# Performance work log

Measured on AMD Instinct MI355X. Metric: run time of the kernel, lower is better.

The kernel has to match this reference:

```python
import jax, jax.numpy as jnp
import numpy as np

T, D_IN, D_OUT, HEADS, FREQ = 2048, 1024, 1024, 8, 10000
DH = D_OUT // HEADS


def absolute_pos(t, d, freq):
    # AP[pos, 2i] = sin(pos / freq**(2i/d)), AP[pos, 2i+1] = cos(...); t even -> all cols filled
    pos = jnp.arange(t, dtype=jnp.float32)[:, None]            # [T,1]
    i = jnp.arange(t // 2, dtype=jnp.float32)[None, :]         # [1,T/2]
    angle = pos / (freq ** (2.0 * i / d))                      # [T,T/2]
    return jnp.stack([jnp.sin(angle), jnp.cos(angle)], axis=-1).reshape(t, t)


def setup_inputs() -> dict:
    key = jax.random.key(0)
    ks = jax.random.split(key, 6)
    s = 0.02
    return {
        "x": jax.random.normal(ks[0], (T, D_IN), jnp.float32),
        "Wq": jax.random.normal(ks[1], (HEADS, DH, D_IN), jnp.float32) * s,
        "Wk": jax.random.normal(ks[2], (HEADS, DH, D_IN), jnp.float32) * s,
        "Wv": jax.random.normal(ks[3], (HEADS, DH, D_IN), jnp.float32) * s,
        "Wout2": jax.random.normal(ks[4], (DH, DH + 2), jnp.float32) * s,
        "Wout": jax.random.normal(ks[5], (D_IN, D_OUT), jnp.float32) * s,
    }


def reference(x, Wq, Wk, Wv, Wout2, Wout):
    t = x.shape[0]
    # diversity = 1 - cosine similarity (F.normalize with eps=1e-12)
    x_unit = x / jnp.maximum(jnp.linalg.norm(x, axis=1, keepdims=True), 1e-12)
    diversity = 1.0 - x_unit @ x_unit.T                        # [T,T]

    # all heads vectorized; torch Linear weight is [out,in] -> x @ W.T
    Q = jnp.einsum('td,hed->hte', x, Wq)                       # [H,T,DH]
    K = jnp.einsum('td,hed->hte', x, Wk)
    V = jnp.einsum('td,hed->hte', x, Wv)

    AP = absolute_pos(t, D_IN, FREQ)                           # [T,T]
    energies = jnp.einsum('hte,hse->hts', Q, K) + AP           # [H,T,T]

    att = jax.nn.softmax(energies, axis=-1)
    logp = jax.nn.log_softmax(energies, axis=-1)
    entropy = -(att * logp).sum(-1) / np.float32(np.log(t))    # [H,T]
    entropy = entropy / jnp.maximum(jnp.abs(entropy).sum(-1, keepdims=True), 1e-12)

    # dep_factor[j] broadcast over rows: masked[i,j] = dep[j]*att[i,j]
    dep = (diversity[None] * att).sum(-1) / diversity.sum(-1)[None]  # [H,T]
    att_win = att + dep[:, None, :] * att                      # [H,T,T]

    # dropout(p=0.5) treated as identity (eval mode)
    y = jnp.einsum('hts,hse->hte', att_win, V)                 # [H,T,DH]

    chars = jax.lax.stop_gradient(jnp.stack([entropy, dep], axis=-1))  # [H,T,2]
    y_s = jnp.einsum('htf,of->hto', jnp.concatenate([y, chars], axis=-1), Wout2)  # [H,T,DH]

    y_cat = jnp.transpose(y_s, (1, 0, 2)).reshape(t, D_OUT)    # cat heads along feature dim
    out = y_cat @ Wout.T                                       # [T,D_IN]
    return out, att_win[-1]
```

## Files before the change

### kernel.cpp

```cpp
#include <hip/hip_runtime.h>
#include <math.h>

#define TT  2048
#define NH  8
#define DH  128
#define LNT 7.6246189861593985f

typedef unsigned short ushort_t;
typedef __bf16 bf16x8 __attribute__((ext_vector_type(8)));
typedef _Float16 f16x8 __attribute__((ext_vector_type(8)));
typedef float f32x4 __attribute__((ext_vector_type(4)));
typedef unsigned int uintx4 __attribute__((ext_vector_type(4)));

#define MFMA16(a, b, c)  __builtin_amdgcn_mfma_f32_16x16x32_bf16(a, b, c, 0, 0, 0)
#define MFMA16F(a, b, c) __builtin_amdgcn_mfma_f32_16x16x32_f16(a, b, c, 0, 0, 0)

__device__ __forceinline__ bf16x8 ld8(const ushort_t* p) {
  uintx4 v = *(const uintx4*)p;
  return __builtin_bit_cast(bf16x8, v);
}
__device__ __forceinline__ f16x8 ld8f(const ushort_t* p) {
  uintx4 v = *(const uintx4*)p;
  return __builtin_bit_cast(f16x8, v);
}
__device__ __forceinline__ ushort_t f2bf(float x) {
  unsigned u = __float_as_uint(x);
  return (ushort_t)((u + 0x7fffu + ((u >> 16) & 1u)) >> 16);
}
__device__ __forceinline__ float bf2f(ushort_t b) {
  return __uint_as_float(((unsigned)b) << 16);
}
__device__ __forceinline__ ushort_t f2h(float x) {
  return __builtin_bit_cast(ushort_t, (_Float16)x);
}
__device__ __forceinline__ float h2f(ushort_t b) {
  return (float)__builtin_bit_cast(_Float16, b);
}


enum : size_t {
  F_XF   = 0u,
  F_UF   = 1048576u,
  F_QF   = 2097152u,
  F_KF   = 3145728u,
  F_VBF  = 4194304u,
  F_VT   = 5242880u,
  F_YCF  = 6291456u,
  F_WCAT = 7340032u,
  F_WOF  = 9437184u,
  F_DIVS = 9961472u,
  F_LST  = 9979904u,
  F_ENTR = 9996288u,
  F_ENT  = 10012672u,
  F_DEP  = 10029056u,
  F_W2F  = 10307584u,
  F_APH  = 10485760u,
  F_C    = 12582912u,
  F_LP   = 6291456u,
  F_SAP  = 6422528u,
  F_SCP  = 6553600u,
  F_E    = 16777216u,
  F_YPALL= 33554432u,
  F_YSH  = 2097152u,
};

__device__ __forceinline__ float blockReduceSum256(float v) {
  __shared__ float sh[4];
  #pragma unroll
  for (int m = 1; m < 64; m <<= 1) v += __shfl_xor(v, m, 64);
  if ((threadIdx.x & 63) == 0) sh[threadIdx.x >> 6] = v;
  __syncthreads();
  float r = sh[0] + sh[1] + sh[2] + sh[3];
  __syncthreads();
  return r;
}

__global__ __launch_bounds__(256) void k_pre(
    const float* __restrict__ x, const float* __restrict__ Wq,
    const float* __restrict__ Wk, const float* __restrict__ Wv,
    const float* __restrict__ Wo, const float* __restrict__ W2,
    ushort_t* __restrict__ xf, ushort_t* __restrict__ Wcat,
    ushort_t* __restrict__ Wof, ushort_t* __restrict__ W2f,
    ushort_t* __restrict__ Uf, float* __restrict__ divsum) {
  int b = blockIdx.x;
  if (b < 6240) {
    int i = b * 256 + threadIdx.x;
    if (i < 1572864) {
      const float* src; ushort_t* dst; int j;
      if (i < 524288)       { src = x;  dst = xf;             j = i; }
      else if (i < 786432)  { src = Wq; dst = Wcat;           j = i - 524288; }
      else if (i < 1048576) { src = Wk; dst = Wcat + 1048576; j = i - 786432; }
      else if (i < 1310720) { src = Wv; dst = Wcat + 2097152; j = i - 1048576; }
      else                  { src = Wo; dst = Wof;            j = i - 1310720; }
      float4 v = ((const float4*)src)[j];
      uint2 w;
      w.x = (unsigned)f2h(v.x) | ((unsigned)f2h(v.y) << 16);
      w.y = (unsigned)f2h(v.z) | ((unsigned)f2h(v.w) << 16);
      ((uint2*)dst)[j] = w;
    } else {
      int idx = i - 1572864;
      int o = idx / 192, c = idx % 192;
      W2f[idx] = (c < 130) ? f2h(W2[o * 130 + c]) : (ushort_t)0;
    }
  } else if (b < 8288) {
    int t = b - 6240;
    const float* xr = x + (size_t)t * 1024;
    float ss = 0.f;
    for (int d = threadIdx.x; d < 1024; d += 256) { float v = xr[d]; ss += v * v; }
    ss = blockReduceSum256(ss);
    float inv = 1.f / fmaxf(sqrtf(ss), 1e-12f);
    for (int d = threadIdx.x; d < 1024; d += 256)
      Uf[(size_t)t * 1024 + d] = f2h(xr[d] * inv);
  } else {
    int idx = (b - 8288) * 256 + threadIdx.x;
    if (idx < TT) divsum[idx] = (float)TT;
  }
}

template <int MODE>
__device__ __forceinline__ void gemm_tile(
    ushort_t* As, ushort_t* Bs,
    const ushort_t* A, const ushort_t* B,
    float* Df, ushort_t* Dh,
    ushort_t* Dq, ushort_t* Dk, ushort_t* Dv,
    int M, int N, int K, int m0, int n0) {
  int tid = threadIdx.x, lane = tid & 63, w = tid >> 6;
  int l15 = lane & 15, lg = lane >> 4;
  int wr = w >> 1, wc = w & 1;

  const ushort_t* ga[4];
  const ushort_t* gb[4];
  ushort_t* la[4];
  ushort_t* lb[4];
  #pragma unroll
  for (int j = 0; j < 4; j++) {
    int u = (4 * w + j) * 64 + lane;
    int row = u >> 3;
    int kc8 = (u & 7) ^ (row & 7);
    ga[j] = A + (size_t)(m0 + row) * K + kc8 * 8;
    gb[j] = B + (size_t)(n0 + row) * K + kc8 * 8;
    la[j] = As + (4 * w + j) * 512;
    lb[j] = Bs + (4 * w + j) * 512;
  }

  f32x4 acc[4][4];
  #pragma unroll
  for (int i = 0; i < 4; i++)
    #pragma unroll
    for (int ct = 0; ct < 4; ct++) acc[i][ct] = (f32x4)0.f;

  for (int k0 = 0; k0 < K; k0 += 64) {
    __syncthreads();
    #pragma unroll
    for (int j = 0; j < 4; j++) {
      __builtin_amdgcn_global_load_lds(
          (const __attribute__((address_space(1))) void*)(ga[j] + k0),
          (__attribute__((address_space(3))) void*)la[j], 16, 0, 0);
      __builtin_amdgcn_global_load_lds(
          (const __attribute__((address_space(1))) void*)(gb[j] + k0),
          (__attribute__((address_space(3))) void*)lb[j], 16, 0, 0);
    }
    __syncthreads();
    #pragma unroll
    for (int kc = 0; kc < 2; kc++) {
      f16x8 af[4], bfr[4];
      #pragma unroll
      for (int i = 0; i < 4; i++) {
        int ra = wr * 64 + i * 16 + l15;
        af[i] = ld8f(As + (ra * 8 + ((kc * 4 + lg) ^ (ra & 7))) * 8);
        int rb = wc * 64 + i * 16 + l15;
        bfr[i] = ld8f(Bs + (rb * 8 + ((kc * 4 + lg) ^ (rb & 7))) * 8);
      }
      #pragma unroll
      for (int i = 0; i < 4; i++)
        #pragma unroll
        for (int ct = 0; ct < 4; ct++)
          acc[i][ct] = MFMA16F(af[i], bfr[ct], acc[i][ct]);
    }
  }
  #pragma unroll
  for (int i = 0; i < 4; i++) {
    float rs[4] = {0.f, 0.f, 0.f, 0.f};
    #pragma unroll
    for (int ct = 0; ct < 4; ct++) {
      if (MODE == 5 || MODE == 6) {
        size_t tile_t = (size_t)(m0 + wr * 64 + i * 16) >> 4;
        size_t tile_s = (size_t)(n0 + wc * 64 + ct * 16) >> 4;
        uint2 wv;
        wv.x = (unsigned)f2bf(acc[i][ct][0]) | ((unsigned)f2bf(acc[i][ct][1]) << 16);
        wv.y = (unsigned)f2bf(acc[i][ct][2]) | ((unsigned)f2bf(acc[i][ct][3]) << 16);
        *(uint2*)(Dh + (tile_t * (size_t)(N >> 4) + tile_s) * 256 + lg * 64 + l15 * 4) = wv;
        if (MODE == 6) {
          rs[0] += acc[i][ct][0]; rs[1] += acc[i][ct][1];
          rs[2] += acc[i][ct][2]; rs[3] += acc[i][ct][3];
        }
      } else {
        #pragma unroll
        for (int r = 0; r < 4; r++) {
          size_t mm = m0 + wr * 64 + i * 16 + lg * 4 + r;
          size_t nn = n0 + wc * 64 + ct * 16 + l15;
          float v = acc[i][ct][r];
          if (MODE == 0) Df[mm * N + nn] = v;
          if (MODE == 3) {
            if (nn < 1024) Dq[mm * 1024 + nn] = f2h(v);
            else if (nn < 2048) Dk[mm * 1024 + nn - 1024] = f2h(v);
            else Dv[mm * 1024 + nn - 2048] = f2bf(v);
          }
          if (MODE == 4) {
            size_t hh = mm >> 11, tt2 = mm & 2047;
            Dh[tt2 * 1024 + hh * 128 + nn] = f2h(v);
          }
        }
      }
    }
    if (MODE == 6) {
      #pragma unroll
      for (int r = 0; r < 4; r++) {
        float s = rs[r];
        s += __shfl_xor(s, 1, 64); s += __shfl_xor(s, 2, 64);
        s += __shfl_xor(s, 4, 64); s += __shfl_xor(s, 8, 64);
        if (l15 == 0)
          atomicAdd(&Df[m0 + wr * 64 + i * 16 + lg * 4 + r], -s);
      }
    }
  }
}

template <int MODE>
__global__ __launch_bounds__(256) void k_gemm(
    const ushort_t* __restrict__ A, const ushort_t* __restrict__ B,
    float* __restrict__ Df, ushort_t* __restrict__ Dh,
    int M, int N, int K) {
  __shared__ __align__(16) ushort_t As[128 * 64];
  __shared__ __align__(16) ushort_t Bs[128 * 64];
  gemm_tile<MODE>(As, Bs, A, B, Df, Dh, nullptr, nullptr, nullptr,
                  M, N, K, blockIdx.y * 128, blockIdx.x * 128);
}

__global__ __launch_bounds__(256) void k_cqkv(
    const ushort_t* __restrict__ Uf, const ushort_t* __restrict__ xf,
    const ushort_t* __restrict__ Wcat,
    ushort_t* __restrict__ Cf, ushort_t* __restrict__ Qf,
    ushort_t* __restrict__ Kf, ushort_t* __restrict__ Vbf,
    float* __restrict__ divsum, ushort_t* __restrict__ APf) {
  __shared__ __align__(16) ushort_t As[128 * 64];
  __shared__ __align__(16) ushort_t Bs[128 * 64];
  int bid = blockIdx.x;
  if (bid < 256) {
    gemm_tile<6>(As, Bs, Uf, Uf, divsum, Cf, nullptr, nullptr, nullptr,
                 TT, TT, 1024, (bid >> 4) * 128, (bid & 15) * 128);
  } else if (bid < 640) {
    int b = bid - 256;
    gemm_tile<3>(As, Bs, xf, Wcat, nullptr, nullptr, Qf, Kf, Vbf,
                 TT, 3072, 1024, (b / 24) * 128, (b % 24) * 128);
  } else {
    int bb = bid - 640;
    int tile_t = bb >> 4, sub = bb & 15;
    int base = sub * 2048;
    for (int u0 = threadIdx.x; u0 < 2048; u0 += 256) {
      int u = base + u0;
      int tile_s = u >> 8, slot = u & 255;
      int lg = slot >> 6, l15 = (slot >> 2) & 15, r = slot & 3;
      int t = tile_t * 16 + lg * 4 + r;
      int s = tile_s * 16 + l15;
      int i = s >> 1;
      float invf = __expf((float)i * -0.017988946039016016f);
      float ang = (float)t * invf;
      APf[(size_t)tile_t * 32768 + u] = f2h((s & 1) ? cosf(ang) : sinf(ang));
    }
  }
}

__global__ __launch_bounds__(512, 4) void k_phase1m(
    const ushort_t* __restrict__ Qf, const ushort_t* __restrict__ Kf,
    const ushort_t* __restrict__ APf, const ushort_t* __restrict__ Cf,
    ushort_t* __restrict__ Ef,
    float* __restrict__ Lp, float* __restrict__ sap, float* __restrict__ scp) {
  int h = blockIdx.y, z = blockIdx.z;
  int tid = threadIdx.x, lane = tid & 63, w = tid >> 6;
  int l15 = lane & 15, lg = lane >> 4;
  int rowbase = blockIdx.x * 128 + w * 16;
  int s_begin = z * 256, s_end = s_begin + 256;
  __shared__ __align__(16) ushort_t Ks[64 * 128];

  f16x8 q[4];
  {
    const ushort_t* qp = Qf + (size_t)(rowbase + l15) * 1024 + h * DH + lg * 8;
    #pragma unroll
    for (int kc = 0; kc < 4; kc++) q[kc] = ld8f(qp + kc * 32);
  }
  const ushort_t* apb = APf + (size_t)(rowbase >> 4) * 32768 + lane * 4;
  const ushort_t* cfb = Cf  + (size_t)(rowbase >> 4) * 32768 + lane * 4;
  ushort_t* eb = Ef + ((size_t)(h * 128 + (rowbase >> 4)) * 128) * 256 + lane * 4;

  int n0 = w * 128 + lane;
  int sr0 = n0 >> 4, su0 = n0 & 15, sr1 = sr0 + 4;
  int wo0 = sr0 * 128 + ((su0 ^ (sr0 & 7)) * 8);
  int wo1 = sr1 * 128 + ((su0 ^ (sr1 & 7)) * 8);
  const ushort_t* kg0 = Kf + (size_t)sr0 * 1024 + h * DH + su0 * 8;
  const ushort_t* kg1 = Kf + (size_t)sr1 * 1024 + h * DH + su0 * 8;

  float Lv[4], sae[4], snc[4];
  #pragma unroll
  for (int r = 0; r < 4; r++) { Lv[r] = 0.f; sae[r] = 0.f; snc[r] = 0.f; }

  uintx4 ka = *(const uintx4*)(kg0 + (size_t)s_begin * 1024);
  uintx4 kb = *(const uintx4*)(kg1 + (size_t)s_begin * 1024);

  for (int s0 = s_begin; s0 < s_end; s0 += 64) {
    int ts0 = s0 >> 4;
    f32x4 acc[4];
    float cc[4][4];
    #pragma unroll
    for (int ct = 0; ct < 4; ct++) {
      uint2 ap2 = *(const uint2*)(apb + (size_t)(ts0 + ct) * 256);
      uint2 c2  = *(const uint2*)(cfb + (size_t)(ts0 + ct) * 256);
      acc[ct][0] = h2f((ushort_t)(ap2.x & 0xffffu));
      acc[ct][1] = h2f((ushort_t)(ap2.x >> 16));
      acc[ct][2] = h2f((ushort_t)(ap2.y & 0xffffu));
      acc[ct][3] = h2f((ushort_t)(ap2.y >> 16));
      cc[ct][0] = bf2f((ushort_t)(c2.x & 0xffffu));
      cc[ct][1] = bf2f((ushort_t)(c2.x >> 16));
      cc[ct][2] = bf2f((ushort_t)(c2.y & 0xffffu));
      cc[ct][3] = bf2f((ushort_t)(c2.y >> 16));
    }
    __syncthreads();
    *(uintx4*)(Ks + wo0) = ka;
    *(uintx4*)(Ks + wo1) = kb;
    int s1 = s0 + 64;
    if (s1 < s_end) {
      ka = *(const uintx4*)(kg0 + (size_t)s1 * 1024);
      kb = *(const uintx4*)(kg1 + (size_t)s1 * 1024);
    }
    __syncthreads();
    #pragma unroll
    for (int ct = 0; ct < 4; ct++) {
      int row = ct * 16 + l15, rb = row * 128, rsw = row & 7;
      #pragma unroll
      for (int kc = 0; kc < 4; kc++) {
        f16x8 b = ld8f(Ks + rb + (((kc * 4 + lg) ^ rsw) * 8));
        acc[ct] = MFMA16F(q[kc], b, acc[ct]);
      }
    }
    #pragma unroll
    for (int ct = 0; ct < 4; ct++) {
      uint2 ev;
      ev.x = (unsigned)f2h(acc[ct][0]) | ((unsigned)f2h(acc[ct][1]) << 16);
      ev.y = (unsigned)f2h(acc[ct][2]) | ((unsigned)f2h(acc[ct][3]) << 16);
      *(uint2*)(eb + (size_t)(ts0 + ct) * 256) = ev;
    }
    #pragma unroll
    for (int r = 0; r < 4; r++) {
      float e0 = acc[0][r], e1 = acc[1][r], e2 = acc[2][r], e3 = acc[3][r];
      float p0 = __expf(e0), p1 = __expf(e1), p2 = __expf(e2), p3 = __expf(e3);
      Lv[r]  += (p0 + p1) + (p2 + p3);
      sae[r] += (p0 * e0 + p1 * e1) + (p2 * e2 + p3 * e3);
      snc[r] += (p0 * cc[0][r] + p1 * cc[1][r]) + (p2 * cc[2][r] + p3 * cc[3][r]);
    }
  }
  #pragma unroll
  for (int r = 0; r < 4; r++) {
    #pragma unroll
    for (int m = 1; m < 16; m <<= 1) {
      Lv[r]  += __shfl_xor(Lv[r], m, 64);
      sae[r] += __shfl_xor(sae[r], m, 64);
      snc[r] += __shfl_xor(snc[r], m, 64);
    }
  }
  if (l15 == 0) {
    #pragma unroll
    for (int r = 0; r < 4; r++) {
      int t = rowbase + lg * 4 + r;
      size_t idx = (size_t)z * (NH * TT) + h * TT + t;
      Lp[idx] = Lv[r]; sap[idx] = sae[r]; scp[idx] = snc[r];
    }
  }
}

__global__ __launch_bounds__(256) void k_combine(
    const float* __restrict__ Lp, const float* __restrict__ sap,
    const float* __restrict__ scp, const float* __restrict__ divsum,
    float* __restrict__ Lst, float* __restrict__ entraw, float* __restrict__ dep) {
  int i = blockIdx.x * 256 + threadIdx.x;
  if (i >= NH * TT) return;
  float L = 0.f, sa = 0.f, sc = 0.f;
  #pragma unroll
  for (int c = 0; c < 8; c++) {
    size_t idx = (size_t)c * (NH * TT) + i;
    L += Lp[idx]; sa += sap[idx]; sc += scp[idx];
  }
  float logL = __logf(L);
  Lst[i] = logL;
  entraw[i] = (logL - sa / L) * (1.0f / LNT);
  int t = i & (TT - 1);
  dep[i] = (1.f - sc / L) / divsum[t];
}

__global__ __launch_bounds__(256) void k_entvp(
    const float* __restrict__ entraw, float* __restrict__ ent,
    const ushort_t* __restrict__ Vbf, const float* __restrict__ dep,
    ushort_t* __restrict__ VT) {
  __shared__ float tile[64][130];
  int b = blockIdx.x;
  if (b < 8) {
    int h = b;
    float s = 0.f;
    for (int t = threadIdx.x; t < TT; t += 256) s += fabsf(entraw[h * TT + t]);
    s = blockReduceSum256(s);
    float inv = 1.f / fmaxf(s, 1e-12f);
    for (int t = threadIdx.x; t < TT; t += 256)
      ent[h * TT + t] = entraw[h * TT + t] * inv;
  } else {
    int bb = b - 8;
    int h = bb >> 5, s0 = (bb & 31) * 64;
    int tid = threadIdx.x;
    for (int idx = tid; idx < 64 * 64; idx += 256) {
      int r = idx >> 6, c2 = (idx & 63) * 2;
      unsigned u = *(const unsigned*)&Vbf[(size_t)(s0 + r) * 1024 + h * DH + c2];
      tile[r][c2] = bf2f((ushort_t)(u & 0xffffu));
      tile[r][c2 + 1] = bf2f((ushort_t)(u >> 16));
    }
    __syncthreads();
    int e = tid >> 1, sh = (tid & 1) * 32;
    #pragma unroll
    for (int g = 0; g < 8; g++) {
      int sb = sh + g * 4;
      float v0 = tile[sb + 0][e] * (1.f + dep[h * TT + s0 + sb + 0]);
      float v1 = tile[sb + 1][e] * (1.f + dep[h * TT + s0 + sb + 1]);
      float v2 = tile[sb + 2][e] * (1.f + dep[h * TT + s0 + sb + 2]);
      float v3 = tile[sb + 3][e] * (1.f + dep[h * TT + s0 + sb + 3]);
      uint2 wv;
      wv.x = (unsigned)f2bf(v0) | ((unsigned)f2bf(v1) << 16);
      wv.y = (unsigned)f2bf(v2) | ((unsigned)f2bf(v3) << 16);
      *(uint2*)&VT[(size_t)(h * DH + e) * TT + s0 + sb] = wv;
    }
  }
}

__global__ __launch_bounds__(512, 4) void k_phase2m(
    const ushort_t* __restrict__ Ef, const ushort_t* __restrict__ VT,
    const float* __restrict__ Lst, const float* __restrict__ dep,
    ushort_t* __restrict__ ypall, float* __restrict__ out2) {
  int h = (blockIdx.y + 7) & 7;
  int z = blockIdx.z;
  int tid = threadIdx.x, lane = tid & 63, w = tid >> 6;
  int l15 = lane & 15, lg = lane >> 4;
  int rowbase = blockIdx.x * 128 + w * 16;
  bool last = (h == NH - 1);
  int s_begin = z * 256, s_end = s_begin + 256;
  ushort_t* yp = ypall + (size_t)z * 2097152;

  __shared__ __align__(16) ushort_t Vs[128 * 64];
  __shared__ __align__(16) ushort_t Pst[8][16][72];

  float ml[4];
  #pragma unroll
  for (int r = 0; r < 4; r++) ml[r] = Lst[h * TT + rowbase + lg * 4 + r];
  const ushort_t* eb = Ef + ((size_t)(h * 128 + (rowbase >> 4)) * 128) * 256 + lane * 4;

  int n0 = w * 128 + lane;
  int ve0 = n0 >> 3, vu0 = n0 & 7;
  int vwo0 = ve0 * 64 + ((vu0 ^ (ve0 & 7)) * 8);
  int vwo1 = vwo0 + 512;
  const ushort_t* vg0 = VT + (size_t)(h * DH + ve0) * TT + vu0 * 8;
  const ushort_t* vg1 = vg0 + (size_t)8 * TT;

  f32x4 yacc[8];
  #pragma unroll
  for (int et = 0; et < 8; et++) yacc[et] = (f32x4)0.f;

  uintx4 va = *(const uintx4*)(vg0 + s_begin);
  uintx4 vb = *(const uintx4*)(vg1 + s_begin);

  for (int s0 = s_begin; s0 < s_end; s0 += 64) {
    int ts0 = s0 >> 4;
    uint2 e2[4];
    #pragma unroll
    for (int ct = 0; ct < 4; ct++)
      e2[ct] = *(const uint2*)(eb + (size_t)(ts0 + ct) * 256);
    __syncthreads();
    *(uintx4*)(Vs + vwo0) = va;
    *(uintx4*)(Vs + vwo1) = vb;
    int s1 = s0 + 64;
    if (s1 < s_end) {
      va = *(const uintx4*)(vg0 + s1);
      vb = *(const uintx4*)(vg1 + s1);
    }
    __syncthreads();
    float dv[4];
    if (last) {
      #pragma unroll
      for (int ct = 0; ct < 4; ct++) dv[ct] = dep[(NH - 1) * TT + s0 + ct * 16 + l15];
    }
    #pragma unroll
    for (int ct = 0; ct < 4; ct++) {
      float e0 = h2f((ushort_t)(e2[ct].x & 0xffffu));
      float e1 = h2f((ushort_t)(e2[ct].x >> 16));
      float e3 = h2f((ushort_t)(e2[ct].y & 0xffffu));
      float e4 = h2f((ushort_t)(e2[ct].y >> 16));
      float a0 = __expf(e0 - ml[0]);
      float a1 = __expf(e1 - ml[1]);
      float a2 = __expf(e3 - ml[2]);
      float a3 = __expf(e4 - ml[3]);
      Pst[w][lg * 4 + 0][ct * 16 + l15] = f2bf(a0);
      Pst[w][lg * 4 + 1][ct * 16 + l15] = f2bf(a1);
      Pst[w][lg * 4 + 2][ct * 16 + l15] = f2bf(a2);
      Pst[w][lg * 4 + 3][ct * 16 + l15] = f2bf(a3);
      if (last) {
        float sc = 1.f + dv[ct];
        out2[(size_t)(rowbase + lg * 4 + 0) * TT + s0 + ct * 16 + l15] = a0 * sc;
        out2[(size_t)(rowbase + lg * 4 + 1) * TT + s0 + ct * 16 + l15] = a1 * sc;
        out2[(size_t)(rowbase + lg * 4 + 2) * TT + s0 + ct * 16 + l15] = a2 * sc;
        out2[(size_t)(rowbase + lg * 4 + 3) * TT + s0 + ct * 16 + l15] = a3 * sc;
      }
    }
    asm volatile("" ::: "memory");
    #pragma unroll
    for (int c = 0; c < 2; c++) {
      bf16x8 ap = *(const bf16x8*)&Pst[w][l15][c * 32 + lg * 8];
      #pragma unroll
      for (int et = 0; et < 8; et++) {
        int e = et * 16 + l15;
        bf16x8 bv = ld8(Vs + e * 64 + (((c * 4 + lg) ^ (l15 & 7)) * 8));
        yacc[et] = MFMA16(ap, bv, yacc[et]);
      }
    }
    asm volatile("" ::: "memory");
  }
  #pragma unroll
  for (int et = 0; et < 8; et++)
    #pragma unroll
    for (int r = 0; r < 4; r++)
      yp[((size_t)h * TT + rowbase + lg * 4 + r) * DH + et * 16 + l15] = f2h(yacc[et][r]);
}

__device__ __forceinline__ void acc8(const ushort_t* p, float* s) {
  uintx4 v = *(const uintx4*)p;
  #pragma unroll
  for (int q = 0; q < 4; q++) {
    s[q * 2]     += h2f((ushort_t)(v[q] & 0xffffu));
    s[q * 2 + 1] += h2f((ushort_t)(v[q] >> 16));
  }
}
__global__ __launch_bounds__(256) void k_ysum(
    const ushort_t* __restrict__ ypall,
    const float* __restrict__ ent, const float* __restrict__ dep,
    ushort_t* __restrict__ ysh) {
  int i = blockIdx.x * 256 + threadIdx.x;
  int g = i & 15, t = (i >> 4) & 2047, h = i >> 15;
  size_t src = ((size_t)h * TT + t) * DH + g * 8;
  float s[8];
  #pragma unroll
  for (int q = 0; q < 8; q++) s[q] = 0.f;
  #pragma unroll
  for (int b = 0; b < 8; b++) acc8(ypall + (size_t)b * 2097152 + src, s);
  uintx4 o;
  o[0] = (unsigned)f2h(s[0]) | ((unsigned)f2h(s[1]) << 16);
  o[1] = (unsigned)f2h(s[2]) | ((unsigned)f2h(s[3]) << 16);
  o[2] = (unsigned)f2h(s[4]) | ((unsigned)f2h(s[5]) << 16);
  o[3] = (unsigned)f2h(s[6]) | ((unsigned)f2h(s[7]) << 16);
  ushort_t* row = ysh + ((size_t)h * TT + t) * 192;
  *(uintx4*)(row + g * 8) = o;
  if (g == 0) {
    uint2 cz;
    cz.x = (unsigned)f2h(ent[h * TT + t]) | ((unsigned)f2h(dep[h * TT + t]) << 16);
    cz.y = 0u;
    *(uint2*)(row + 128) = cz;
    uint2 z2; z2.x = 0u; z2.y = 0u;
    #pragma unroll
    for (int q = 132; q < 192; q += 4) *(uint2*)(row + q) = z2;
  }
}

extern "C" void kernel_launch(void* const* d_in, const int* in_sizes, int n_in,
                              void* d_out, int out_size, void* d_ws, size_t ws_size,
                              hipStream_t stream) {
  const float* x  = (const float*)d_in[0];
  const float* Wq = (const float*)d_in[1];
  const float* Wk = (const float*)d_in[2];
  const float* Wv = (const float*)d_in[3];
  const float* W2 = (const float*)d_in[4];
  const float* Wo = (const float*)d_in[5];
  float* out  = (float*)d_out;
  float* out2 = out + (size_t)TT * 1024;
  float* ws = (float*)d_ws;

  ushort_t* xf   = (ushort_t*)(ws + F_XF);
  ushort_t* Uf   = (ushort_t*)(ws + F_UF);
  ushort_t* Qf   = (ushort_t*)(ws + F_QF);
  ushort_t* Kf   = (ushort_t*)(ws + F_KF);
  ushort_t* Vbf  = (ushort_t*)(ws + F_VBF);
  ushort_t* VT   = (ushort_t*)(ws + F_VT);
  ushort_t* ycf  = (ushort_t*)(ws + F_YCF);
  ushort_t* Wcat = (ushort_t*)(ws + F_WCAT);
  ushort_t* Wof  = (ushort_t*)(ws + F_WOF);
  ushort_t* W2f  = (ushort_t*)(ws + F_W2F);
  ushort_t* APf  = (ushort_t*)(ws + F_APH);
  ushort_t* ysh  = (ushort_t*)(ws + F_YSH);
  ushort_t* Cf   = (ushort_t*)(ws + F_C);
  ushort_t* Ef   = (ushort_t*)(ws + F_E);
  ushort_t* ypall= (ushort_t*)(ws + F_YPALL);
  float* divsum = ws + F_DIVS;
  float* Lst    = ws + F_LST;
  float* entraw = ws + F_ENTR;
  float* ent    = ws + F_ENT;
  float* dep    = ws + F_DEP;
  float* Lp     = ws + F_LP;
  float* sap    = ws + F_SAP;
  float* scp    = ws + F_SCP;

  k_pre<<<8296, 256, 0, stream>>>(x, Wq, Wk, Wv, Wo, W2,
                                  xf, Wcat, Wof, W2f, Uf, divsum);
  k_cqkv<<<2688, 256, 0, stream>>>(Uf, xf, Wcat, Cf, Qf, Kf, Vbf, divsum, APf);

  k_phase1m<<<dim3(16, NH, 8), 512, 0, stream>>>(Qf, Kf, APf, Cf, Ef, Lp, sap, scp);
  k_combine<<<64, 256, 0, stream>>>(Lp, sap, scp, divsum, Lst, entraw, dep);
  k_entvp<<<264, 256, 0, stream>>>(entraw, ent, Vbf, dep, VT);
  k_phase2m<<<dim3(16, NH, 8), 512, 0, stream>>>(Ef, VT, Lst, dep, ypall, out2);
  k_ysum<<<1024, 256, 0, stream>>>(ypall, ent, dep, ysh);
  k_gemm<4><<<dim3(1, 128), 256, 0, stream>>>(ysh, W2f, nullptr, ycf, 16384, 128, 192);
  k_gemm<0><<<dim3(8, 16), 256, 0, stream>>>(ycf, Wof, out, nullptr, TT, 1024, 1024);
}
```

Measured before the change: 158.2 us.

## Exploit symmetry of cosine-similarity Gram matrix and fuse x conversion into norm pass

The U·Uᵀ Gram tile GEMM now computes only the upper-triangular 128x128 tiles (136 instead of 256 blocks). Each off-diagonal tile also writes its transpose into the tiled bf16 buffer and adds its column sums into the row-sum accumulator. Separately, the fp16 conversion of x moves into the row-normalisation blocks, so x is read once for both outputs. This removes about half the MFMA work of the diversity GEMM, at the cost of scattered 2-byte transposed stores and extra atomics.

```diff
diff --git a/kernel.cpp b/kernel.cpp
--- a/kernel.cpp
+++ b/kernel.cpp
@@ -83,36 +83,38 @@
     ushort_t* __restrict__ Wof, ushort_t* __restrict__ W2f,
     ushort_t* __restrict__ Uf, float* __restrict__ divsum) {
   int b = blockIdx.x;
-  if (b < 6240) {
+  if (b < 4192) {
     int i = b * 256 + threadIdx.x;
-    if (i < 1572864) {
+    if (i < 1048576) {
       const float* src; ushort_t* dst; int j;
-      if (i < 524288)       { src = x;  dst = xf;             j = i; }
-      else if (i < 786432)  { src = Wq; dst = Wcat;           j = i - 524288; }
-      else if (i < 1048576) { src = Wk; dst = Wcat + 1048576; j = i - 786432; }
-      else if (i < 1310720) { src = Wv; dst = Wcat + 2097152; j = i - 1048576; }
-      else                  { src = Wo; dst = Wof;            j = i - 1310720; }
+      if (i < 262144)       { src = Wq; dst = Wcat;           j = i; }
+      else if (i < 524288)  { src = Wk; dst = Wcat + 1048576; j = i - 262144; }
+      else if (i < 786432)  { src = Wv; dst = Wcat + 2097152; j = i - 524288; }
+      else                  { src = Wo; dst = Wof;            j = i - 786432; }
       float4 v = ((const float4*)src)[j];
       uint2 w;
       w.x = (unsigned)f2h(v.x) | ((unsigned)f2h(v.y) << 16);
       w.y = (unsigned)f2h(v.z) | ((unsigned)f2h(v.w) << 16);
       ((uint2*)dst)[j] = w;
     } else {
-      int idx = i - 1572864;
+      int idx = i - 1048576;
       int o = idx / 192, c = idx % 192;
       W2f[idx] = (c < 130) ? f2h(W2[o * 130 + c]) : (ushort_t)0;
     }
-  } else if (b < 8288) {
-    int t = b - 6240;
+  } else if (b < 6240) {
+    int t = b - 4192;
     const float* xr = x + (size_t)t * 1024;
     float ss = 0.f;
     for (int d = threadIdx.x; d < 1024; d += 256) { float v = xr[d]; ss += v * v; }
     ss = blockReduceSum256(ss);
     float inv = 1.f / fmaxf(sqrtf(ss), 1e-12f);
-    for (int d = threadIdx.x; d < 1024; d += 256)
-      Uf[(size_t)t * 1024 + d] = f2h(xr[d] * inv);
+    for (int d = threadIdx.x; d < 1024; d += 256) {
+      float v = xr[d];
+      Uf[(size_t)t * 1024 + d] = f2h(v * inv);
+      xf[(size_t)t * 1024 + d] = f2h(v);
+    }
   } else {
-    int idx = (b - 8288) * 256 + threadIdx.x;
+    int idx = (b - 6240) * 256 + threadIdx.x;
     if (idx < TT) divsum[idx] = (float)TT;
   }
 }
@@ -178,23 +180,61 @@
           acc[i][ct] = MFMA16F(af[i], bfr[ct], acc[i][ct]);
     }
   }
-  #pragma unroll
-  for (int i = 0; i < 4; i++) {
-    float rs[4] = {0.f, 0.f, 0.f, 0.f};
-    #pragma unroll
-    for (int ct = 0; ct < 4; ct++) {
-      if (MODE == 5 || MODE == 6) {
+  if (MODE == 7) {
+    #pragma unroll
+    for (int i = 0; i < 4; i++) {
+      float rs[4] = {0.f, 0.f, 0.f, 0.f};
+      #pragma unroll
+      for (int ct = 0; ct < 4; ct++) {
         size_t tile_t = (size_t)(m0 + wr * 64 + i * 16) >> 4;
         size_t tile_s = (size_t)(n0 + wc * 64 + ct * 16) >> 4;
         uint2 wv;
         wv.x = (unsigned)f2bf(acc[i][ct][0]) | ((unsigned)f2bf(acc[i][ct][1]) << 16);
         wv.y = (unsigned)f2bf(acc[i][ct][2]) | ((unsigned)f2bf(acc[i][ct][3]) << 16);
         *(uint2*)(Dh + (tile_t * (size_t)(N >> 4) + tile_s) * 256 + lg * 64 + l15 * 4) = wv;
-        if (MODE == 6) {
-          rs[0] += acc[i][ct][0]; rs[1] += acc[i][ct][1];
-          rs[2] += acc[i][ct][2]; rs[3] += acc[i][ct][3];
+        rs[0] += acc[i][ct][0]; rs[1] += acc[i][ct][1];
+        rs[2] += acc[i][ct][2]; rs[3] += acc[i][ct][3];
+      }
+      #pragma unroll
+      for (int r = 0; r < 4; r++) {
+        float s = rs[r];
+        s += __shfl_xor(s, 1, 64); s += __shfl_xor(s, 2, 64);
+        s += __shfl_xor(s, 4, 64); s += __shfl_xor(s, 8, 64);
+        if (l15 == 0)
+          atomicAdd(&Df[m0 + wr * 64 + i * 16 + lg * 4 + r], -s);
+      }
+    }
+    if (m0 != n0) {
+      #pragma unroll
+      for (int ct = 0; ct < 4; ct++) {
+        float cs = 0.f;
+        #pragma unroll
+        for (int i = 0; i < 4; i++)
+          #pragma unroll
+          for (int r = 0; r < 4; r++) cs += acc[i][ct][r];
+        cs += __shfl_xor(cs, 16, 64);
+        cs += __shfl_xor(cs, 32, 64);
+        if (lane < 16)
+          atomicAdd(&Df[n0 + wc * 64 + ct * 16 + l15], -cs);
+      }
+      #pragma unroll
+      for (int i = 0; i < 4; i++) {
+        #pragma unroll
+        for (int ct = 0; ct < 4; ct++) {
+          size_t mbase = (((size_t)(n0 + wc * 64 + ct * 16) >> 4) * (size_t)(N >> 4)
+                          + ((size_t)(m0 + wr * 64 + i * 16) >> 4)) * 256;
+          #pragma unroll
+          for (int r = 0; r < 4; r++)
+            Dh[mbase + (l15 >> 2) * 64 + (lg * 4 + r) * 4 + (l15 & 3)] =
+                f2bf(acc[i][ct][r]);
         }
-      } else {
+      }
+    }
+  } else {
+    #pragma unroll
+    for (int i = 0; i < 4; i++) {
+      #pragma unroll
+      for (int ct = 0; ct < 4; ct++) {
         #pragma unroll
         for (int r = 0; r < 4; r++) {
           size_t mm = m0 + wr * 64 + i * 16 + lg * 4 + r;
@@ -213,16 +253,6 @@
         }
       }
     }
-    if (MODE == 6) {
-      #pragma unroll
-      for (int r = 0; r < 4; r++) {
-        float s = rs[r];
-        s += __shfl_xor(s, 1, 64); s += __shfl_xor(s, 2, 64);
-        s += __shfl_xor(s, 4, 64); s += __shfl_xor(s, 8, 64);
-        if (l15 == 0)
-          atomicAdd(&Df[m0 + wr * 64 + i * 16 + lg * 4 + r], -s);
-      }
-    }
   }
 }
 
@@ -246,15 +276,18 @@
   __shared__ __align__(16) ushort_t As[128 * 64];
   __shared__ __align__(16) ushort_t Bs[128 * 64];
   int bid = blockIdx.x;
-  if (bid < 256) {
-    gemm_tile<6>(As, Bs, Uf, Uf, divsum, Cf, nullptr, nullptr, nullptr,
-                 TT, TT, 1024, (bid >> 4) * 128, (bid & 15) * 128);
-  } else if (bid < 640) {
-    int b = bid - 256;
+  if (bid < 136) {
+    int rem = bid, bt = 0;
+    while (rem >= 16 - bt) { rem -= 16 - bt; ++bt; }
+    int bs = bt + rem;
+    gemm_tile<7>(As, Bs, Uf, Uf, divsum, Cf, nullptr, nullptr, nullptr,
+                 TT, TT, 1024, bt * 128, bs * 128);
+  } else if (bid < 520) {
+    int b = bid - 136;
     gemm_tile<3>(As, Bs, xf, Wcat, nullptr, nullptr, Qf, Kf, Vbf,
                  TT, 3072, 1024, (b / 24) * 128, (b % 24) * 128);
   } else {
-    int bb = bid - 640;
+    int bb = bid - 520;
     int tile_t = bb >> 4, sub = bb & 15;
     int base = sub * 2048;
     for (int u0 = threadIdx.x; u0 < 2048; u0 += 256) {
@@ -609,9 +642,9 @@
   float* sap    = ws + F_SAP;
   float* scp    = ws + F_SCP;
 
-  k_pre<<<8296, 256, 0, stream>>>(x, Wq, Wk, Wv, Wo, W2,
+  k_pre<<<6248, 256, 0, stream>>>(x, Wq, Wk, Wv, Wo, W2,
                                   xf, Wcat, Wof, W2f, Uf, divsum);
-  k_cqkv<<<2688, 256, 0, stream>>>(Uf, xf, Wcat, Cf, Qf, Kf, Vbf, divsum, APf);
+  k_cqkv<<<2568, 256, 0, stream>>>(Uf, xf, Wcat, Cf, Qf, Kf, Vbf, divsum, APf);
 
   k_phase1m<<<dim3(16, NH, 8), 512, 0, stream>>>(Qf, Kf, APf, Cf, Ef, Lp, sap, scp);
   k_combine<<<64, 256, 0, stream>>>(Lp, sap, scp, divsum, Lst, entraw, dep);
```

After: 157.6 us. No clear change (-0.4%).
